# Kernel optimization log

Hardware: AMD Instinct MI355X
Metric: run time of the kernel (lower is better)

Reference implementation:

```python
import jax, jax.numpy as jnp
import numpy as np
import math

B, S, D = 4, 2048, 1024

def setup_inputs() -> dict:
    key = jax.random.key(0)
    k_x, k_q, k_k, k_v = jax.random.split(key, 4)
    scale = 1.0 / math.sqrt(D)
    return {
        "x": jax.random.normal(k_x, (B, S, D), dtype=jnp.float32),
        "W_Q": jax.random.normal(k_q, (D, D), dtype=jnp.float32) * scale,
        "W_K": jax.random.normal(k_k, (D, D), dtype=jnp.float32) * scale,
        "W_V": jax.random.normal(k_v, (D, D), dtype=jnp.float32) * scale,
    }

def reference(x, W_Q, W_K, W_V):
    # nn.Linear(bias=False): y = x @ W.T
    Q = jnp.einsum('bsd,ed->bse', x, W_Q)
    K = jnp.einsum('bsd,ed->bse', x, W_K)
    V = jnp.einsum('bsd,ed->bse', x, W_V)
    scores = jnp.einsum('bqd,bkd->bqk', Q, K) / jnp.sqrt(jnp.asarray(Q.shape[-1], Q.dtype))
    weight = jax.nn.softmax(scores, axis=-1)  # [B,S,S]
    return jnp.einsum('bqk,bkd->bqd', weight, V)
```

## Files before the change

### kernel.cpp

```cpp
#include <hip/hip_runtime.h>
#include <stdint.h>

typedef __bf16 bf16;
typedef __bf16 bf16x8 __attribute__((ext_vector_type(8)));
typedef __bf16 bf16x4 __attribute__((ext_vector_type(4)));
typedef float f32x4 __attribute__((ext_vector_type(4)));

__device__ inline void gload_lds16(const void* g, void* l) {
  __builtin_amdgcn_global_load_lds(
      (__attribute__((address_space(1))) void*)g,
      (__attribute__((address_space(3))) void*)l, 16, 0, 0);
}

__device__ inline void xcd_swizzle(int& bx, int& by, int& bz) {
  const int gx = gridDim.x, gy = gridDim.y;
  int lin = blockIdx.x + gx * (blockIdx.y + gy * blockIdx.z);
  const int nwg = gx * gy * gridDim.z;
  lin = (lin & 7) * (nwg >> 3) + (lin >> 3);
  bx = lin % gx;
  const int tmp = lin / gx;
  by = tmp % gy;
  bz = tmp / gy;
}

__global__ __launch_bounds__(256) void cvt_all(
    const float* __restrict__ x, const float* __restrict__ wq,
    const float* __restrict__ wk, const float* __restrict__ wv,
    bf16* __restrict__ xb2, bf16* __restrict__ Wb2) {
  const int NX = 2097152;
  const int NW = 262144;
  int i = blockIdx.x * 256 + threadIdx.x;
  const int stride = gridDim.x * 256;
  for (int p = i; p < NX + 3 * NW; p += stride) {
    const float* src; bf16* dst; int off;
    if (p < NX) {
      src = x; off = p;
      const int row = p >> 8, c4 = p & 255;
      dst = xb2 + ((long)row << 11) + (c4 << 2);
    } else {
      int q = p - NX; const int w = q >> 18; off = q & (NW - 1);
      src = (w == 0) ? wq : ((w == 1) ? wk : wv);
      const int row = off >> 8, c4 = off & 255;
      dst = Wb2 + ((long)(w * 1024 + row) << 11) + (c4 << 2);
    }
    float4 v = ((const float4*)src)[off];
    bf16x4 o;
    o[0] = (bf16)v.x; o[1] = (bf16)v.y; o[2] = (bf16)v.z; o[3] = (bf16)v.w;
    *(bf16x4*)dst = o;
  }
}

__global__ __launch_bounds__(512, 2) void gemm8(
    const bf16* __restrict__ Ag, const bf16* __restrict__ Bg,
    bf16* __restrict__ Cg,
    long lda, long ldb, long ldc,
    long sA, long sB, long sC, int K, float scale)
{
  constexpr int BUFSZ = 65536;
  __shared__ alignas(16) char lds[2 * BUFSZ];
  int bx, by, bz;
  xcd_swizzle(bx, by, bz);
  const int tid = threadIdx.x;
  const int l = tid & 63;
  const int wv = tid >> 6;
  const int fr = l & 15;
  const int kch = l >> 4;
  const int m0 = by * 256;
  const int n0 = bx * 256;
  const bf16* Ab = Ag + (long)bz * sA;
  const bf16* Bb = Bg + (long)bz * sB;

  const int wm = wv >> 2;
  const int wn = wv & 3;

  const int a_rd = fr * 128 + (((wm * 4 + kch) ^ (fr & 7)) << 4);
  const int b_rd = (wn & 1) * 8192 + fr * 128 + ((((wn >> 1) * 4 + kch) ^ (fr & 7)) << 4);

  const int se = (tid & 7) ^ ((tid >> 3) & 7);
  const int s_row = (se >> 2) * 128 + (tid >> 3);
  const int s_k = (se & 3) * 8;
  const int wb16 = (tid & 448) * 16;

  const int NT = K >> 6;
  f32x4 acc[8][4] = {};

  auto stageA = [&](int tile, int kh, int buf) {
#pragma unroll
    for (int rd = 0; rd < 2; ++rd)
      gload_lds16(Ab + (long)(m0 + s_row + rd * 64) * lda + tile * 64 + kh * 32 + s_k,
                  lds + buf * BUFSZ + kh * 16384 + rd * 8192 + wb16);
  };
  auto stageB = [&](int tile, int kh, int buf) {
#pragma unroll
    for (int rd = 0; rd < 2; ++rd)
      gload_lds16(Bb + (long)(n0 + s_row + rd * 64) * ldb + tile * 64 + kh * 32 + s_k,
                  lds + buf * BUFSZ + 32768 + kh * 16384 + rd * 8192 + wb16);
  };

  stageA(0, 0, 0); stageB(0, 0, 0); stageA(0, 1, 0); stageB(0, 1, 0);
  stageA(min(1, NT - 1), 0, 1); stageB(min(1, NT - 1), 0, 1);
  asm volatile("s_waitcnt vmcnt(4)" ::: "memory");
  __builtin_amdgcn_sched_barrier(0);
  __builtin_amdgcn_s_barrier();

  for (int t = 0; t < NT; ++t) {
    const char* bufA = lds + (t & 1) * BUFSZ;
    const char* bufB = bufA + 32768;
    const int t1 = min(t + 1, NT - 1);
    const int t2 = min(t + 2, NT - 1);
    const int nb = (t & 1) ^ 1;
    const int cur = t & 1;

    bf16x8 bfg[4], af[4];
    stageA(t1, 1, nb);
#pragma unroll
    for (int n = 0; n < 4; ++n) bfg[n] = *(const bf16x8*)(bufB + n * 2048 + b_rd);
#pragma unroll
    for (int m = 0; m < 4; ++m) af[m] = *(const bf16x8*)(bufA + m * 2048 + a_rd);
    __builtin_amdgcn_s_setprio(1);
#pragma unroll
    for (int m = 0; m < 4; ++m)
#pragma unroll
      for (int n = 0; n < 4; ++n)
        acc[m][n] = __builtin_amdgcn_mfma_f32_16x16x32_bf16(af[m], bfg[n], acc[m][n], 0, 0, 0);
    __builtin_amdgcn_s_setprio(0);
    __builtin_amdgcn_s_barrier();
    stageB(t1, 1, nb);
#pragma unroll
    for (int m = 0; m < 4; ++m) af[m] = *(const bf16x8*)(bufA + 8192 + m * 2048 + a_rd);
    __builtin_amdgcn_s_setprio(1);
#pragma unroll
    for (int m = 0; m < 4; ++m)
#pragma unroll
      for (int n = 0; n < 4; ++n)
        acc[4 + m][n] = __builtin_amdgcn_mfma_f32_16x16x32_bf16(af[m], bfg[n], acc[4 + m][n], 0, 0, 0);
    __builtin_amdgcn_s_setprio(0);
    __builtin_amdgcn_s_barrier();
    stageA(t2, 0, cur);
#pragma unroll
    for (int n = 0; n < 4; ++n) bfg[n] = *(const bf16x8*)(bufB + 16384 + n * 2048 + b_rd);
#pragma unroll
    for (int m = 0; m < 4; ++m) af[m] = *(const bf16x8*)(bufA + 16384 + m * 2048 + a_rd);
    __builtin_amdgcn_s_setprio(1);
#pragma unroll
    for (int m = 0; m < 4; ++m)
#pragma unroll
      for (int n = 0; n < 4; ++n)
        acc[m][n] = __builtin_amdgcn_mfma_f32_16x16x32_bf16(af[m], bfg[n], acc[m][n], 0, 0, 0);
    __builtin_amdgcn_s_setprio(0);
    __builtin_amdgcn_s_barrier();
    stageB(t2, 0, cur);
#pragma unroll
    for (int m = 0; m < 4; ++m) af[m] = *(const bf16x8*)(bufA + 16384 + 8192 + m * 2048 + a_rd);
    __builtin_amdgcn_s_setprio(1);
#pragma unroll
    for (int m = 0; m < 4; ++m)
#pragma unroll
      for (int n = 0; n < 4; ++n)
        acc[4 + m][n] = __builtin_amdgcn_mfma_f32_16x16x32_bf16(af[m], bfg[n], acc[4 + m][n], 0, 0, 0);
    __builtin_amdgcn_s_setprio(0);
    asm volatile("s_waitcnt vmcnt(4)" ::: "memory");
    __builtin_amdgcn_sched_barrier(0);
    __builtin_amdgcn_s_barrier();
  }
  asm volatile("s_waitcnt vmcnt(0)" ::: "memory");

#pragma unroll
  for (int mf = 0; mf < 8; ++mf) {
    const int row = m0 + wm * 128 + (mf >> 2) * 64 + (mf & 3) * 16 + (l >> 4) * 4;
#pragma unroll
    for (int n = 0; n < 4; ++n) {
      const int col = n0 + wn * 64 + n * 16 + fr;
      bf16* C = Cg + (long)bz * sC;
#pragma unroll
      for (int r = 0; r < 4; ++r)
        C[(long)(row + r) * ldc + col] = (bf16)(acc[mf][n][r] * scale);
    }
  }
}

__global__ __launch_bounds__(512, 2) void projV(
    const bf16* __restrict__ Xg, const bf16* __restrict__ Wv,
    bf16* __restrict__ Vt)
{
  constexpr int BUFSZ = 49152;
  __shared__ alignas(16) char lds[2 * BUFSZ];
  int bx, by, bz;
  xcd_swizzle(bx, by, bz);
  const int tid = threadIdx.x;
  const int l = tid & 63;
  const int wv = tid >> 6;
  const int wm = wv >> 2;
  const int wn = wv & 3;
  const int fr = l & 15;
  const int kch = l >> 4;
  const int m0 = by * 256;
  const int n0 = bx * 128;
  const bf16* Xb = Xg + (long)bz * 4194304;

  const int a_rd = fr * 128 + (((wm * 4 + kch) ^ (fr & 7)) << 4);
  int b_off[2];
#pragma unroll
  for (int n = 0; n < 2; ++n)
    b_off[n] = 32768 + ((wn & 1) * 32 + n * 16 + fr) * 128 +
               ((((wn >> 1) * 4 + kch) ^ (fr & 7)) << 4);

  const int se = (tid & 7) ^ ((tid >> 3) & 7);
  const int s_rowA = (se >> 2) * 128 + (tid >> 3);
  const int s_rowB = (se >> 2) * 64 + (tid >> 3);
  const int s_k = (se & 3) * 8;
  const int wb16 = (tid & 448) * 16;

  const int NT = 16;
  f32x4 acc[8][2] = {};

  auto stageA = [&](int tile, int kh, int buf) {
#pragma unroll
    for (int rd = 0; rd < 2; ++rd)
      gload_lds16(Xb + (long)(m0 + s_rowA + rd * 64) * 2048 + tile * 64 + kh * 32 + s_k,
                  lds + buf * BUFSZ + kh * 16384 + rd * 8192 + wb16);
  };
  auto stageB = [&](int tile, int kh, int buf) {
    gload_lds16(Wv + (long)(n0 + s_rowB) * 2048 + tile * 64 + kh * 32 + s_k,
                lds + buf * BUFSZ + 32768 + kh * 8192 + wb16);
  };

  stageA(0, 0, 0); stageB(0, 0, 0); stageA(0, 1, 0); stageB(0, 1, 0);
  stageA(1, 0, 1); stageB(1, 0, 1);
  asm volatile("s_waitcnt vmcnt(3)" ::: "memory");
  __builtin_amdgcn_sched_barrier(0);
  __builtin_amdgcn_s_barrier();

  for (int t = 0; t < NT; ++t) {
    const char* bufA = lds + (t & 1) * BUFSZ;
    const int t1 = min(t + 1, NT - 1);
    const int t2 = min(t + 2, NT - 1);
    const int nb = (t & 1) ^ 1;
    const int cur = t & 1;

    bf16x8 bfg[2], af[4];
    stageA(t1, 1, nb);
#pragma unroll
    for (int n = 0; n < 2; ++n) bfg[n] = *(const bf16x8*)(bufA + b_off[n]);
#pragma unroll
    for (int m = 0; m < 4; ++m) af[m] = *(const bf16x8*)(bufA + m * 2048 + a_rd);
    __builtin_amdgcn_s_setprio(1);
#pragma unroll
    for (int m = 0; m < 4; ++m)
#pragma unroll
      for (int n = 0; n < 2; ++n)
        acc[m][n] = __builtin_amdgcn_mfma_f32_16x16x32_bf16(af[m], bfg[n], acc[m][n], 0, 0, 0);
    __builtin_amdgcn_s_setprio(0);
    __builtin_amdgcn_s_barrier();
    stageB(t1, 1, nb);
#pragma unroll
    for (int m = 0; m < 4; ++m) af[m] = *(const bf16x8*)(bufA + 8192 + m * 2048 + a_rd);
    __builtin_amdgcn_s_setprio(1);
#pragma unroll
    for (int m = 0; m < 4; ++m)
#pragma unroll
      for (int n = 0; n < 2; ++n)
        acc[4 + m][n] = __builtin_amdgcn_mfma_f32_16x16x32_bf16(af[m], bfg[n], acc[4 + m][n], 0, 0, 0);
    __builtin_amdgcn_s_setprio(0);
    __builtin_amdgcn_s_barrier();
    stageA(t2, 0, cur);
#pragma unroll
    for (int n = 0; n < 2; ++n) bfg[n] = *(const bf16x8*)(bufA + 8192 + b_off[n]);
#pragma unroll
    for (int m = 0; m < 4; ++m) af[m] = *(const bf16x8*)(bufA + 16384 + m * 2048 + a_rd);
    __builtin_amdgcn_s_setprio(1);
#pragma unroll
    for (int m = 0; m < 4; ++m)
#pragma unroll
      for (int n = 0; n < 2; ++n)
        acc[m][n] = __builtin_amdgcn_mfma_f32_16x16x32_bf16(af[m], bfg[n], acc[m][n], 0, 0, 0);
    __builtin_amdgcn_s_setprio(0);
    __builtin_amdgcn_s_barrier();
    stageB(t2, 0, cur);
#pragma unroll
    for (int m = 0; m < 4; ++m) af[m] = *(const bf16x8*)(bufA + 16384 + 8192 + m * 2048 + a_rd);
    __builtin_amdgcn_s_setprio(1);
#pragma unroll
    for (int m = 0; m < 4; ++m)
#pragma unroll
      for (int n = 0; n < 2; ++n)
        acc[4 + m][n] = __builtin_amdgcn_mfma_f32_16x16x32_bf16(af[m], bfg[n], acc[4 + m][n], 0, 0, 0);
    __builtin_amdgcn_s_setprio(0);
    asm volatile("s_waitcnt vmcnt(3)" ::: "memory");
    __builtin_amdgcn_sched_barrier(0);
    __builtin_amdgcn_s_barrier();
  }
  asm volatile("s_waitcnt vmcnt(0)" ::: "memory");

#pragma unroll
  for (int mf = 0; mf < 8; ++mf) {
    const int s = m0 + wm * 128 + (mf >> 2) * 64 + (mf & 3) * 16 + (l >> 4) * 4;
#pragma unroll
    for (int n = 0; n < 2; ++n) {
      const int d = n0 + wn * 32 + n * 16 + fr;
      bf16x4 pk;
#pragma unroll
      for (int r = 0; r < 4; ++r) pk[r] = (bf16)acc[mf][n][r];
      *(bf16x4*)(Vt + (long)bz * 2097152 + (long)d * 2048 + s) = pk;
    }
  }
}

__global__ __launch_bounds__(256, 2) void gemm2h(
    const bf16* __restrict__ Ag, const bf16* __restrict__ Bg,
    float* __restrict__ Cg,
    long lda, long ldb, long ldc,
    long sA, long sB, long sC, int K)
{
  constexpr int BUFSZ = 32768;
  __shared__ alignas(16) char lds[2 * BUFSZ];
  int bx, by, bz;
  xcd_swizzle(bx, by, bz);
  const int tid = threadIdx.x;
  const int l = tid & 63;
  const int wv = tid >> 6;
  const int wm = wv >> 1, wn = wv & 1;
  const int fr = l & 15;
  const int kch = l >> 4;
  const int m0 = by * 128;
  const int n0 = bx * 128;
  const bf16* Ab = Ag + (long)bz * sA;
  const bf16* Bb = Bg + (long)bz * sB;

  const int a_rd = fr * 128 + (((wm * 4 + kch) ^ (fr & 7)) << 4);
  const int b_rd = fr * 128 + (((wn * 4 + kch) ^ (fr & 7)) << 4);

  const int se = (tid & 7) ^ ((tid >> 3) & 7);
  const int s_row = (se >> 2) * 64 + (tid >> 3);
  const int s_k = (se & 3) * 8;
  const int wb16 = (tid >> 6) * 1024;

  const int NT = K >> 6;
  f32x4 acc[4][4] = {};

  auto stageA = [&](int tile, int kh, int buf) {
#pragma unroll
    for (int rd = 0; rd < 2; ++rd)
      gload_lds16(Ab + (long)(m0 + s_row + rd * 32) * lda + tile * 64 + kh * 32 + s_k,
                  lds + buf * BUFSZ + kh * 8192 + rd * 4096 + wb16);
  };
  auto stageB = [&](int tile, int kh, int buf) {
#pragma unroll
    for (int rd = 0; rd < 2; ++rd)
      gload_lds16(Bb + (long)(n0 + s_row + rd * 32) * ldb + tile * 64 + kh * 32 + s_k,
                  lds + buf * BUFSZ + 16384 + kh * 8192 + rd * 4096 + wb16);
  };

  stageA(0, 0, 0); stageB(0, 0, 0); stageA(0, 1, 0); stageB(0, 1, 0);
  stageA(min(1, NT - 1), 0, 1); stageB(min(1, NT - 1), 0, 1);
  asm volatile("s_waitcnt vmcnt(4)" ::: "memory");
  __builtin_amdgcn_sched_barrier(0);
  __builtin_amdgcn_s_barrier();

  for (int t = 0; t < NT; ++t) {
    const char* bufA = lds + (t & 1) * BUFSZ;
    const char* bufB = bufA + 16384;
    const int t1 = min(t + 1, NT - 1);
    const int t2 = min(t + 2, NT - 1);
    const int nb = (t & 1) ^ 1;
    const int cur = t & 1;

    bf16x8 bfg[4], af[4];
    stageA(t1, 1, nb); stageB(t1, 1, nb);
#pragma unroll
    for (int n = 0; n < 4; ++n) bfg[n] = *(const bf16x8*)(bufB + n * 2048 + b_rd);
#pragma unroll
    for (int m = 0; m < 4; ++m) af[m] = *(const bf16x8*)(bufA + m * 2048 + a_rd);
    __builtin_amdgcn_s_setprio(1);
#pragma unroll
    for (int m = 0; m < 4; ++m)
#pragma unroll
      for (int n = 0; n < 4; ++n)
        acc[m][n] = __builtin_amdgcn_mfma_f32_16x16x32_bf16(af[m], bfg[n], acc[m][n], 0, 0, 0);
    __builtin_amdgcn_s_setprio(0);
    __builtin_amdgcn_s_barrier();
    stageA(t2, 0, cur); stageB(t2, 0, cur);
#pragma unroll
    for (int n = 0; n < 4; ++n) bfg[n] = *(const bf16x8*)(bufB + 8192 + n * 2048 + b_rd);
#pragma unroll
    for (int m = 0; m < 4; ++m) af[m] = *(const bf16x8*)(bufA + 8192 + m * 2048 + a_rd);
    __builtin_amdgcn_s_setprio(1);
#pragma unroll
    for (int m = 0; m < 4; ++m)
#pragma unroll
      for (int n = 0; n < 4; ++n)
        acc[m][n] = __builtin_amdgcn_mfma_f32_16x16x32_bf16(af[m], bfg[n], acc[m][n], 0, 0, 0);
    __builtin_amdgcn_s_setprio(0);
    asm volatile("s_waitcnt vmcnt(4)" ::: "memory");
    __builtin_amdgcn_sched_barrier(0);
    __builtin_amdgcn_s_barrier();
  }
  asm volatile("s_waitcnt vmcnt(0)" ::: "memory");

#pragma unroll
  for (int mf = 0; mf < 4; ++mf) {
    const int row = m0 + wm * 64 + mf * 16 + (l >> 4) * 4;
#pragma unroll
    for (int n = 0; n < 4; ++n) {
      const int col = n0 + wn * 64 + n * 16 + fr;
      float* C = Cg + (long)bz * sC;
#pragma unroll
      for (int r = 0; r < 4; ++r)
        C[(long)(row + r) * ldc + col] = acc[mf][n][r];
    }
  }
}

__global__ __launch_bounds__(256) void softmax_k(const bf16* __restrict__ Sm,
                                                 bf16* __restrict__ P, int cols) {
  __shared__ float red[8];
  const long row = blockIdx.x;
  const bf16* sr = Sm + row * (long)cols;
  bf16* pr = P + row * (long)cols;
  const int t = threadIdx.x;
  bf16x8 v = *(const bf16x8*)(sr + t * 8);
  float e[8];
#pragma unroll
  for (int j = 0; j < 8; ++j) e[j] = (float)v[j];
  float m = e[0];
#pragma unroll
  for (int j = 1; j < 8; ++j) m = fmaxf(m, e[j]);
#pragma unroll
  for (int o = 32; o; o >>= 1) m = fmaxf(m, __shfl_xor(m, o));
  if ((t & 63) == 0) red[t >> 6] = m;
  __syncthreads();
  m = fmaxf(fmaxf(red[0], red[1]), fmaxf(red[2], red[3]));
  float s = 0.f;
#pragma unroll
  for (int j = 0; j < 8; ++j) { e[j] = __expf(e[j] - m); s += e[j]; }
#pragma unroll
  for (int o = 32; o; o >>= 1) s += __shfl_xor(s, o);
  if ((t & 63) == 0) red[4 + (t >> 6)] = s;
  __syncthreads();
  s = red[4] + red[5] + red[6] + red[7];
  const float inv = 1.0f / s;
  bf16x8 o8;
#pragma unroll
  for (int j = 0; j < 8; ++j) o8[j] = (bf16)(e[j] * inv);
  *(bf16x8*)(pr + t * 8) = o8;
}

extern "C" void kernel_launch(void* const* d_in, const int* in_sizes, int n_in,
                              void* d_out, int out_size, void* d_ws, size_t ws_size,
                              hipStream_t stream) {
  const float* x  = (const float*)d_in[0];
  const float* Wq = (const float*)d_in[1];
  const float* Wk = (const float*)d_in[2];
  const float* Wv = (const float*)d_in[3];
  float* out = (float*)d_out;

  char* ws = (char*)d_ws;
  bf16* QKbuf = (bf16*)(ws);
  bf16* P     = (bf16*)(ws);
  bf16* Vt    = (bf16*)(ws + 33554432);
  bf16* scb   = (bf16*)(ws + 50331648);
  bf16* xb2   = (bf16*)(ws + 50331648);
  bf16* Wb2   = (bf16*)(ws + 83886080);

  dim3 b256(256, 1, 1), b512(512, 1, 1);

  cvt_all<<<2048, b256, 0, stream>>>(x, Wq, Wk, Wv, xb2, Wb2);

  gemm8<<<dim3(8, 8, 4), b512, 0, stream>>>(
      xb2, Wb2, QKbuf, 2048, 2048, 2048,
      4194304, 0, 4194304, 1024, 1.f);

  projV<<<dim3(8, 8, 4), b512, 0, stream>>>(xb2, Wb2 + 2 * 1024 * 2048, Vt);

  gemm8<<<dim3(8, 8, 4), b512, 0, stream>>>(
      QKbuf, QKbuf + 1024, scb, 2048, 2048, 2048,
      4194304, 4194304, 4194304, 1024, 0.03125f);

  softmax_k<<<8192, b256, 0, stream>>>(scb, P, 2048);

  gemm2h<<<dim3(8, 16, 4), b256, 0, stream>>>(
      P, Vt, out, 2048, 2048, 1024,
      4194304, 2097152, 2097152, 2048);
}
```

Baseline: 171.5 us.

## Replace PV GEMM with split-K 256x256 tile GEMM using atomic accumulation

The final P·V product now runs through the larger 256x256-tile gemm8 kernel instead of the 128x128 gemm2h. K is split in two halves across the z grid dimension, and the partial results are accumulated into the fp32 output with atomicAdd. The output is zeroed with a memset beforehand. This raises data reuse per tile while keeping enough workgroups, at the cost of an extra memset, atomic traffic on the output, and nondeterministic summation order.

```diff
diff --git a/kernel.cpp b/kernel.cpp
--- a/kernel.cpp
+++ b/kernel.cpp
@@ -50,9 +50,10 @@
   }
 }
 
+template <int MODE>
 __global__ __launch_bounds__(512, 2) void gemm8(
     const bf16* __restrict__ Ag, const bf16* __restrict__ Bg,
-    bf16* __restrict__ Cg,
+    void* __restrict__ Cg,
     long lda, long ldb, long ldc,
     long sA, long sB, long sC, int K, float scale)
 {
@@ -60,6 +61,8 @@
   __shared__ alignas(16) char lds[2 * BUFSZ];
   int bx, by, bz;
   xcd_swizzle(bx, by, bz);
+  int ks = 0;
+  if constexpr (MODE == 1) { ks = bz & 1; bz >>= 1; }
   const int tid = threadIdx.x;
   const int l = tid & 63;
   const int wv = tid >> 6;
@@ -67,8 +70,8 @@
   const int kch = l >> 4;
   const int m0 = by * 256;
   const int n0 = bx * 256;
-  const bf16* Ab = Ag + (long)bz * sA;
-  const bf16* Bb = Bg + (long)bz * sB;
+  const bf16* Ab = Ag + (long)bz * sA + (long)ks * 1024;
+  const bf16* Bb = Bg + (long)bz * sB + (long)ks * 1024;
 
   const int wm = wv >> 2;
   const int wn = wv & 3;
@@ -171,10 +174,17 @@
 #pragma unroll
     for (int n = 0; n < 4; ++n) {
       const int col = n0 + wn * 64 + n * 16 + fr;
-      bf16* C = Cg + (long)bz * sC;
-#pragma unroll
-      for (int r = 0; r < 4; ++r)
-        C[(long)(row + r) * ldc + col] = (bf16)(acc[mf][n][r] * scale);
+      if constexpr (MODE == 0) {
+        bf16* C = (bf16*)Cg + (long)bz * sC;
+#pragma unroll
+        for (int r = 0; r < 4; ++r)
+          C[(long)(row + r) * ldc + col] = (bf16)(acc[mf][n][r] * scale);
+      } else {
+        float* C = (float*)Cg + (long)bz * sC;
+#pragma unroll
+        for (int r = 0; r < 4; ++r)
+          atomicAdd(&C[(long)(row + r) * ldc + col], acc[mf][n][r]);
+      }
     }
   }
 }
@@ -306,111 +316,6 @@
   }
 }
 
-__global__ __launch_bounds__(256, 2) void gemm2h(
-    const bf16* __restrict__ Ag, const bf16* __restrict__ Bg,
-    float* __restrict__ Cg,
-    long lda, long ldb, long ldc,
-    long sA, long sB, long sC, int K)
-{
-  constexpr int BUFSZ = 32768;
-  __shared__ alignas(16) char lds[2 * BUFSZ];
-  int bx, by, bz;
-  xcd_swizzle(bx, by, bz);
-  const int tid = threadIdx.x;
-  const int l = tid & 63;
-  const int wv = tid >> 6;
-  const int wm = wv >> 1, wn = wv & 1;
-  const int fr = l & 15;
-  const int kch = l >> 4;
-  const int m0 = by * 128;
-  const int n0 = bx * 128;
-  const bf16* Ab = Ag + (long)bz * sA;
-  const bf16* Bb = Bg + (long)bz * sB;
-
-  const int a_rd = fr * 128 + (((wm * 4 + kch) ^ (fr & 7)) << 4);
-  const int b_rd = fr * 128 + (((wn * 4 + kch) ^ (fr & 7)) << 4);
-
-  const int se = (tid & 7) ^ ((tid >> 3) & 7);
-  const int s_row = (se >> 2) * 64 + (tid >> 3);
-  const int s_k = (se & 3) * 8;
-  const int wb16 = (tid >> 6) * 1024;
-
-  const int NT = K >> 6;
-  f32x4 acc[4][4] = {};
-
-  auto stageA = [&](int tile, int kh, int buf) {
-#pragma unroll
-    for (int rd = 0; rd < 2; ++rd)
-      gload_lds16(Ab + (long)(m0 + s_row + rd * 32) * lda + tile * 64 + kh * 32 + s_k,
-                  lds + buf * BUFSZ + kh * 8192 + rd * 4096 + wb16);
-  };
-  auto stageB = [&](int tile, int kh, int buf) {
-#pragma unroll
-    for (int rd = 0; rd < 2; ++rd)
-      gload_lds16(Bb + (long)(n0 + s_row + rd * 32) * ldb + tile * 64 + kh * 32 + s_k,
-                  lds + buf * BUFSZ + 16384 + kh * 8192 + rd * 4096 + wb16);
-  };
-
-  stageA(0, 0, 0); stageB(0, 0, 0); stageA(0, 1, 0); stageB(0, 1, 0);
-  stageA(min(1, NT - 1), 0, 1); stageB(min(1, NT - 1), 0, 1);
-  asm volatile("s_waitcnt vmcnt(4)" ::: "memory");
-  __builtin_amdgcn_sched_barrier(0);
-  __builtin_amdgcn_s_barrier();
-
-  for (int t = 0; t < NT; ++t) {
-    const char* bufA = lds + (t & 1) * BUFSZ;
-    const char* bufB = bufA + 16384;
-    const int t1 = min(t + 1, NT - 1);
-    const int t2 = min(t + 2, NT - 1);
-    const int nb = (t & 1) ^ 1;
-    const int cur = t & 1;
-
-    bf16x8 bfg[4], af[4];
-    stageA(t1, 1, nb); stageB(t1, 1, nb);
-#pragma unroll
-    for (int n = 0; n < 4; ++n) bfg[n] = *(const bf16x8*)(bufB + n * 2048 + b_rd);
-#pragma unroll
-    for (int m = 0; m < 4; ++m) af[m] = *(const bf16x8*)(bufA + m * 2048 + a_rd);
-    __builtin_amdgcn_s_setprio(1);
-#pragma unroll
-    for (int m = 0; m < 4; ++m)
-#pragma unroll
-      for (int n = 0; n < 4; ++n)
-        acc[m][n] = __builtin_amdgcn_mfma_f32_16x16x32_bf16(af[m], bfg[n], acc[m][n], 0, 0, 0);
-    __builtin_amdgcn_s_setprio(0);
-    __builtin_amdgcn_s_barrier();
-    stageA(t2, 0, cur); stageB(t2, 0, cur);
-#pragma unroll
-    for (int n = 0; n < 4; ++n) bfg[n] = *(const bf16x8*)(bufB + 8192 + n * 2048 + b_rd);
-#pragma unroll
-    for (int m = 0; m < 4; ++m) af[m] = *(const bf16x8*)(bufA + 8192 + m * 2048 + a_rd);
-    __builtin_amdgcn_s_setprio(1);
-#pragma unroll
-    for (int m = 0; m < 4; ++m)
-#pragma unroll
-      for (int n = 0; n < 4; ++n)
-        acc[m][n] = __builtin_amdgcn_mfma_f32_16x16x32_bf16(af[m], bfg[n], acc[m][n], 0, 0, 0);
-    __builtin_amdgcn_s_setprio(0);
-    asm volatile("s_waitcnt vmcnt(4)" ::: "memory");
-    __builtin_amdgcn_sched_barrier(0);
-    __builtin_amdgcn_s_barrier();
-  }
-  asm volatile("s_waitcnt vmcnt(0)" ::: "memory");
-
-#pragma unroll
-  for (int mf = 0; mf < 4; ++mf) {
-    const int row = m0 + wm * 64 + mf * 16 + (l >> 4) * 4;
-#pragma unroll
-    for (int n = 0; n < 4; ++n) {
-      const int col = n0 + wn * 64 + n * 16 + fr;
-      float* C = Cg + (long)bz * sC;
-#pragma unroll
-      for (int r = 0; r < 4; ++r)
-        C[(long)(row + r) * ldc + col] = acc[mf][n][r];
-    }
-  }
-}
-
 __global__ __launch_bounds__(256) void softmax_k(const bf16* __restrict__ Sm,
                                                  bf16* __restrict__ P, int cols) {
   __shared__ float red[8];
@@ -464,21 +369,23 @@
 
   dim3 b256(256, 1, 1), b512(512, 1, 1);
 
+  hipMemsetAsync(out, 0, 33554432, stream);
+
   cvt_all<<<2048, b256, 0, stream>>>(x, Wq, Wk, Wv, xb2, Wb2);
 
-  gemm8<<<dim3(8, 8, 4), b512, 0, stream>>>(
+  gemm8<0><<<dim3(8, 8, 4), b512, 0, stream>>>(
       xb2, Wb2, QKbuf, 2048, 2048, 2048,
       4194304, 0, 4194304, 1024, 1.f);
 
   projV<<<dim3(8, 8, 4), b512, 0, stream>>>(xb2, Wb2 + 2 * 1024 * 2048, Vt);
 
-  gemm8<<<dim3(8, 8, 4), b512, 0, stream>>>(
+  gemm8<0><<<dim3(8, 8, 4), b512, 0, stream>>>(
       QKbuf, QKbuf + 1024, scb, 2048, 2048, 2048,
       4194304, 4194304, 4194304, 1024, 0.03125f);
 
   softmax_k<<<8192, b256, 0, stream>>>(scb, P, 2048);
 
-  gemm2h<<<dim3(8, 16, 4), b256, 0, stream>>>(
+  gemm8<1><<<dim3(4, 8, 8), b512, 0, stream>>>(
       P, Vt, out, 2048, 2048, 1024,
-      4194304, 2097152, 2097152, 2048);
-}
+      4194304, 2097152, 2097152, 1024, 1.f);
+}
```

New measurement: 213.4 us. +24.4%, slower.
